# Performance work log

Hardware: AMD Instinct MI355X
Metric: run time of the kernel (lower is better)

The kernel has to match this reference:

```python
import jax, jax.numpy as jnp
import numpy as np

G = 56      # voxel grid side
N = 60000   # active voxels
K = 27      # 3x3x3 kernel offsets
CIN, COUT = 64, 96


def _build_kernel_map(seed=0):
    """Host-side hash-map neighbor search (what spnn does internally).
    Returns in_idx/out_idx of shape (K, N); padded entries have out_idx == N
    (scattered into a trash row) and in_idx == 0 (any valid gather index)."""
    rng = np.random.default_rng(seed)
    flat = rng.choice(G ** 3, size=N, replace=False)
    coords = np.stack(np.unravel_index(flat, (G, G, G)), axis=1)  # (N, 3)
    lut = -np.ones(G ** 3, dtype=np.int64)
    lut[flat] = np.arange(N)
    offs = np.array([(dx, dy, dz) for dx in (-1, 0, 1)
                     for dy in (-1, 0, 1) for dz in (-1, 0, 1)])
    in_idx = np.zeros((K, N), dtype=np.int32)
    out_idx = np.full((K, N), N, dtype=np.int32)
    for k in range(K):
        nb = coords + offs[k]
        ok = np.all((nb >= 0) & (nb < G), axis=1)
        fl = np.clip(nb[:, 0] * G * G + nb[:, 1] * G + nb[:, 2], 0, G ** 3 - 1)
        j = np.where(ok, lut[fl], -1)
        sel = np.nonzero(j >= 0)[0]
        m = sel.shape[0]
        out_idx[k, :m] = sel.astype(np.int32)       # output point i
        in_idx[k, :m] = j[sel].astype(np.int32)     # its neighbor at offset k
    return jnp.asarray(in_idx), jnp.asarray(out_idx)


def setup_inputs() -> dict:
    key = jax.random.key(0)
    ks = jax.random.split(key, 10)
    in_idx, out_idx = _build_kernel_map(0)
    s1 = 1.0 / np.sqrt(K * CIN)
    s2 = 1.0 / np.sqrt(K * COUT)
    return {
        "x":  jax.random.normal(ks[0], (N, CIN), jnp.float32),
        "W1": jax.random.normal(ks[1], (K, CIN, COUT), jnp.float32) * s1,
        "g1": jnp.ones((COUT,), jnp.float32),
        "b1": jnp.zeros((COUT,), jnp.float32),
        "m1": jax.random.normal(ks[2], (COUT,), jnp.float32) * 0.1,
        "v1": jax.random.uniform(ks[3], (COUT,), jnp.float32, 0.5, 1.5),
        "W2": jax.random.normal(ks[4], (K, COUT, COUT), jnp.float32) * s2,
        "g2": jnp.ones((COUT,), jnp.float32),
        "b2": jnp.zeros((COUT,), jnp.float32),
        "m2": jax.random.normal(ks[5], (COUT,), jnp.float32) * 0.1,
        "v2": jax.random.uniform(ks[6], (COUT,), jnp.float32, 0.5, 1.5),
        "Wd": jax.random.normal(ks[7], (CIN, COUT), jnp.float32) / np.sqrt(CIN),
        "gd": jnp.ones((COUT,), jnp.float32),
        "bd": jnp.zeros((COUT,), jnp.float32),
        "md": jax.random.normal(ks[8], (COUT,), jnp.float32) * 0.1,
        "vd": jax.random.uniform(ks[9], (COUT,), jnp.float32, 0.5, 1.5),
        "in_idx": in_idx,
        "out_idx": out_idx,
    }


def _bn(h, g, b, m, v, eps=1e-5):
    return (h - m) * (g * jax.lax.rsqrt(v + eps)) + b


def _sparse_conv(feat, W, in_idx, out_idx):
    # gather -> GEMM -> scatter-add, one pass per kernel offset.
    n = feat.shape[0]
    out = jnp.zeros((n + 1, W.shape[2]), feat.dtype)  # row n = trash row
    for k in range(W.shape[0]):
        out = out.at[out_idx[k]].add(feat[in_idx[k]] @ W[k])
    return out[:n]


def reference(x, W1, g1, b1, m1, v1, W2, g2, b2, m2, v2,
              Wd, gd, bd, md, vd, in_idx, out_idx):
    h = jax.nn.relu(_bn(_sparse_conv(x, W1, in_idx, out_idx), g1, b1, m1, v1))
    h = _bn(_sparse_conv(h, W2, in_idx, out_idx), g2, b2, m2, v2)
    skip = _bn(x @ Wd, gd, bd, md, vd)  # 1x1 conv downsample (inc != outc)
    return jax.nn.relu(h + skip)
```

## Files before the change

### kernel.cpp

```cpp
#include <hip/hip_runtime.h>


typedef __attribute__((ext_vector_type(8))) short bf16x8;
typedef __attribute__((ext_vector_type(4))) float f32x4;
typedef unsigned short u16;

constexpr int K27  = 27;
constexpr int KPAD = 30;
constexpr int CIN  = 64;
constexpr int COUT = 96;
constexpr int W1SZ = 6144;
constexpr int W2SZ = 9216;

#define MFMA __builtin_amdgcn_mfma_f32_16x16x32_bf16

__device__ __forceinline__ u16 f2bf(float f) {
  unsigned u = __float_as_uint(f);
  return (u16)((u + 0x7FFFu + ((u >> 16) & 1u)) >> 16);
}

__device__ __forceinline__ int posf(int c) {
  return ((c >> 2) & 3) * 8 + (c & 3) + ((c >> 4) & 1) * 4;
}

__device__ __forceinline__ bf16x8 ld16(const u16* p) {
  union { bf16x8 f; uint4 u; } r;
  r.u = *reinterpret_cast<const uint4*>(p);
  return r.f;
}

__device__ __forceinline__ void gll(const u16* g, u16* l) {
  __builtin_amdgcn_global_load_lds(
      (const __attribute__((address_space(1))) unsigned int*)g,
      (__attribute__((address_space(3))) unsigned int*)l, 16, 0, 0);
}

__device__ __forceinline__ void stage1(const u16* g, u16* l, int t) {
#pragma unroll
  for (int s = 0; s < 3; ++s) gll(g + s * 2048 + t * 8, l + s * 2048 + t * 8);
}

__device__ __forceinline__ void stage2(const u16* g, u16* l, int t) {
#pragma unroll
  for (int s = 0; s < 4; ++s) gll(g + s * 2048 + t * 8, l + s * 2048 + t * 8);
  if (t < 128) gll(g + 8192 + t * 8, l + 8192 + t * 8);
}

__device__ __forceinline__ int xcd_swz(int bid, int nblk) {
  int q = nblk >> 3, r = nblk & 7;
  int x = bid & 7, i = bid >> 3;
  return (x < r ? x * (q + 1) : r * (q + 1) + (x - r) * q) + i;
}

__global__ void build_nbT(const int* __restrict__ in_idx, const int* __restrict__ out_idx,
                          int* __restrict__ nbT, int N, int N_pad) {
  int t = blockIdx.x * blockDim.x + threadIdx.x;
  if (t >= K27 * N) return;
  int k = t / N;
  int o = out_idx[t];
  if (o < N) nbT[(size_t)k * N_pad + o] = in_idx[t];
}

__global__ void prep_all(
    const float* __restrict__ x, const float* __restrict__ W1,
    const float* __restrict__ W2, const float* __restrict__ Wd,
    const float* g1, const float* b1, const float* m1, const float* v1,
    const float* g2, const float* b2, const float* m2, const float* v2,
    const float* gd, const float* bd, const float* md, const float* vd,
    u16* __restrict__ xbf, u16* __restrict__ W1t, u16* __restrict__ W2t,
    u16* __restrict__ Wdt, float* __restrict__ bnc, u16* __restrict__ hbf, int N) {
  long i = (long)blockIdx.x * blockDim.x + threadIdx.x;
  const long R0 = (long)(N + 1) * CIN;
  const long R1 = (long)K27 * W1SZ;
  const long R2 = (long)K27 * W2SZ;
  const long R3 = (long)CIN * COUT;
  if (i < R0) {
    int c = (int)(i & 63);
    float v = (i < (long)N * CIN) ? x[i] : 0.f;
    xbf[(i & ~63L) + (c & 32) + posf(c & 31)] = f2bf(v);
    return;
  }
  i -= R0;
  if (i < R1) {
    int k = (int)(i / W1SZ), r = (int)(i % W1SZ);
    int f = r >> 9, lane = (r >> 3) & 63, j = r & 7;
    int c = f / 6, n = f % 6, m = lane & 15, g = lane >> 4;
    int co = n * 16 + m;
    int ci = c * 32 + 4 * g + (j & 3) + 16 * (j >> 2);
    W1t[i] = f2bf(W1[((size_t)k * CIN + ci) * COUT + co]);
    return;
  }
  i -= R1;
  if (i < R2) {
    int k = (int)(i / W2SZ), r = (int)(i % W2SZ);
    int f = r >> 9, lane = (r >> 3) & 63, j = r & 7;
    int c = f / 6, n = f % 6, m = lane & 15, g = lane >> 4;
    int co = n * 16 + m;
    int ci = c * 32 + 4 * g + (j & 3) + 16 * (j >> 2);
    W2t[i] = f2bf(W2[((size_t)k * COUT + ci) * COUT + co]);
    return;
  }
  i -= R2;
  if (i < R3) {
    int ci = (int)(i / COUT), co = (int)(i % COUT);
    Wdt[co * CIN + (ci & 32) + posf(ci & 31)] = f2bf(Wd[i]);
    return;
  }
  i -= R3;
  if (i < COUT) {
    int c = (int)i;
    float A1 = g1[c] * rsqrtf(v1[c] + 1e-5f);
    float A2 = g2[c] * rsqrtf(v2[c] + 1e-5f);
    float Ad = gd[c] * rsqrtf(vd[c] + 1e-5f);
    bnc[c]       = A1;
    bnc[96 + c]  = b1[c] - m1[c] * A1;
    bnc[192 + c] = A2;
    bnc[288 + c] = b2[c] - m2[c] * A2 + bd[c] - md[c] * Ad;
    bnc[384 + c] = Ad / A2;
    hbf[(size_t)N * COUT + c] = 0;
  }
}

__global__ __launch_bounds__(256, 2) void conv1_mfma(
    const u16* __restrict__ xbf, const u16* __restrict__ W1t,
    const int* __restrict__ nbT, const float* __restrict__ bnc,
    u16* __restrict__ hbf, int N, int N_pad) {
  __shared__ u16 Blds[2][W1SZ];
  const int t    = threadIdx.x;
  const int lane = t & 63;
  const int m    = lane & 15;
  const int slot = lane >> 4;
  const int so   = slot * 8;
  const int wid  = t >> 6;
  const int wr   = wid >> 1;
  const int wc   = wid & 1;
  const int bswz = xcd_swz(blockIdx.x, gridDim.x);
  const int roww = bswz * 64 + wr * 32;

  f32x4 acc[2][3];
#pragma unroll
  for (int s = 0; s < 2; ++s)
#pragma unroll
    for (int n = 0; n < 3; ++n) acc[s][n] = (f32x4){0.f, 0.f, 0.f, 0.f};

  const int* nbp = nbT + roww + m;

  stage1(W1t, Blds[0], t);
  __builtin_amdgcn_sched_barrier(0);
  int j1a, j1b, j2a, j2b;
  bf16x8 Aa[2][2], Ab[2][2];
  {
    int j0a = nbp[0], j0b = nbp[16];
    j1a = nbp[N_pad];               j1b = nbp[N_pad + 16];
    j2a = nbp[2 * (size_t)N_pad];   j2b = nbp[2 * (size_t)N_pad + 16];
    const u16* pa = xbf + (size_t)(j0a < 0 ? N : j0a) * CIN + so;
    const u16* pb = xbf + (size_t)(j0b < 0 ? N : j0b) * CIN + so;
    Aa[0][0] = ld16(pa); Aa[0][1] = ld16(pa + 32);
    Aa[1][0] = ld16(pb); Aa[1][1] = ld16(pb + 32);
  }
  asm volatile("s_waitcnt vmcnt(6)" ::: "memory");
  __builtin_amdgcn_s_barrier();
  __builtin_amdgcn_sched_barrier(0);

  auto step = [&](int k, bf16x8 (&Ac)[2][2], bf16x8 (&An)[2][2]) {
    const int cur = k & 1;
    stage1(W1t + (size_t)(k + 1) * W1SZ, Blds[cur ^ 1], t);
    __builtin_amdgcn_sched_barrier(0);
    {
      const u16* pa = xbf + (size_t)(j1a < 0 ? N : j1a) * CIN + so;
      const u16* pb = xbf + (size_t)(j1b < 0 ? N : j1b) * CIN + so;
      An[0][0] = ld16(pa); An[0][1] = ld16(pa + 32);
      An[1][0] = ld16(pb); An[1][1] = ld16(pb + 32);
    }
    int j3a = nbp[(size_t)(k + 3) * N_pad];
    int j3b = nbp[(size_t)(k + 3) * N_pad + 16];
    j1a = j2a; j1b = j2b; j2a = j3a; j2b = j3b;
    const u16* Bb = Blds[cur] + wc * 1536 + lane * 8;
#pragma unroll
    for (int c = 0; c < 2; ++c)
#pragma unroll
      for (int nn = 0; nn < 3; ++nn) {
        bf16x8 B = ld16(Bb + (c * 6 + nn) * 512);
        acc[0][nn] = MFMA(Ac[0][c], B, acc[0][nn], 0, 0, 0);
        acc[1][nn] = MFMA(Ac[1][c], B, acc[1][nn], 0, 0, 0);
      }
    asm volatile("s_waitcnt vmcnt(6)" ::: "memory");
    __builtin_amdgcn_s_barrier();
    __builtin_amdgcn_sched_barrier(0);
  };

  for (int kk = 0; kk < K27 - 1; kk += 2) {
    step(kk, Aa, Ab);
    step(kk + 1, Ab, Aa);
  }
  step(K27 - 1, Aa, Ab);
  asm volatile("" :: "v"(Ab[0][0]), "v"(Ab[0][1]), "v"(Ab[1][0]), "v"(Ab[1][1]),
                     "v"(j1a), "v"(j1b), "v"(j2a), "v"(j2b));

  const int pbase = ((m >> 2) << 3) + (m & 3);
#pragma unroll
  for (int nn = 0; nn < 3; ++nn) {
    const int n   = wc * 3 + nn;
    const int col = n * 16 + m;
    const int dcol = (n >> 1) * 32 + pbase + ((n & 1) << 2);
    const float sc = bnc[col], bi = bnc[COUT + col];
#pragma unroll
    for (int s = 0; s < 2; ++s)
#pragma unroll
      for (int r = 0; r < 4; ++r) {
        const int row = roww + s * 16 + slot * 4 + r;
        if (row < N)
          hbf[(size_t)row * COUT + dcol] = f2bf(fmaxf(fmaf(acc[s][nn][r], sc, bi), 0.f));
      }
  }
}

__global__ __launch_bounds__(256, 2) void conv2_mfma(
    const u16* __restrict__ hbf, const u16* __restrict__ W2t,
    const u16* __restrict__ xbf, const u16* __restrict__ Wdt,
    const int* __restrict__ nbT, const float* __restrict__ bnc,
    float* __restrict__ out, int N, int N_pad) {
  __shared__ u16 Blds[2][W2SZ];
  const int t    = threadIdx.x;
  const int lane = t & 63;
  const int m    = lane & 15;
  const int slot = lane >> 4;
  const int so   = slot * 8;
  const int wid  = t >> 6;
  const int wr   = wid >> 1;
  const int wc   = wid & 1;
  const int bswz = xcd_swz(blockIdx.x, gridDim.x);
  const int roww = bswz * 64 + wr * 32;

  f32x4 acc[2][3];
#pragma unroll
  for (int s = 0; s < 2; ++s)
#pragma unroll
    for (int n = 0; n < 3; ++n) acc[s][n] = (f32x4){0.f, 0.f, 0.f, 0.f};

  stage2(W2t, Blds[0], t);
  __builtin_amdgcn_sched_barrier(0);
  {
    int r0 = roww + m, r1 = roww + 16 + m;
    const u16* pa = xbf + (size_t)(r0 < N ? r0 : N) * CIN + so;
    const u16* pb = xbf + (size_t)(r1 < N ? r1 : N) * CIN + so;
    bf16x8 S0a = ld16(pa), S1a = ld16(pa + 32);
    bf16x8 S0b = ld16(pb), S1b = ld16(pb + 32);
#pragma unroll
    for (int nn = 0; nn < 3; ++nn) {
      const int col = (wc * 3 + nn) * 16 + m;
      const u16* wd = Wdt + col * CIN + so;
      bf16x8 B0 = ld16(wd), B1 = ld16(wd + 32);
      acc[0][nn] = MFMA(S0a, B0, acc[0][nn], 0, 0, 0);
      acc[0][nn] = MFMA(S1a, B1, acc[0][nn], 0, 0, 0);
      acc[1][nn] = MFMA(S0b, B0, acc[1][nn], 0, 0, 0);
      acc[1][nn] = MFMA(S1b, B1, acc[1][nn], 0, 0, 0);
    }
#pragma unroll
    for (int nn = 0; nn < 3; ++nn) {
      float rr = bnc[384 + (wc * 3 + nn) * 16 + m];
      acc[0][nn] *= rr;
      acc[1][nn] *= rr;
    }
  }

  const int* nbp = nbT + roww + m;
  int j1a, j1b, j2a, j2b;
  bf16x8 Aa[2][3], Ab[2][3];
  {
    int j0a = nbp[0], j0b = nbp[16];
    j1a = nbp[N_pad];               j1b = nbp[N_pad + 16];
    j2a = nbp[2 * (size_t)N_pad];   j2b = nbp[2 * (size_t)N_pad + 16];
    const u16* pa = hbf + (size_t)(j0a < 0 ? N : j0a) * COUT + so;
    const u16* pb = hbf + (size_t)(j0b < 0 ? N : j0b) * COUT + so;
    Aa[0][0] = ld16(pa); Aa[0][1] = ld16(pa + 32); Aa[0][2] = ld16(pa + 64);
    Aa[1][0] = ld16(pb); Aa[1][1] = ld16(pb + 32); Aa[1][2] = ld16(pb + 64);
  }
  asm volatile("s_waitcnt vmcnt(8)" ::: "memory");
  __builtin_amdgcn_s_barrier();
  __builtin_amdgcn_sched_barrier(0);

  auto step = [&](int k, bf16x8 (&Ac)[2][3], bf16x8 (&An)[2][3]) {
    const int cur = k & 1;
    stage2(W2t + (size_t)(k + 1) * W2SZ, Blds[cur ^ 1], t);
    __builtin_amdgcn_sched_barrier(0);
    {
      const u16* pa = hbf + (size_t)(j1a < 0 ? N : j1a) * COUT + so;
      const u16* pb = hbf + (size_t)(j1b < 0 ? N : j1b) * COUT + so;
      An[0][0] = ld16(pa); An[0][1] = ld16(pa + 32); An[0][2] = ld16(pa + 64);
      An[1][0] = ld16(pb); An[1][1] = ld16(pb + 32); An[1][2] = ld16(pb + 64);
    }
    int j3a = nbp[(size_t)(k + 3) * N_pad];
    int j3b = nbp[(size_t)(k + 3) * N_pad + 16];
    j1a = j2a; j1b = j2b; j2a = j3a; j2b = j3b;
    const u16* Bb = Blds[cur] + wc * 1536 + lane * 8;
#pragma unroll
    for (int c = 0; c < 3; ++c)
#pragma unroll
      for (int nn = 0; nn < 3; ++nn) {
        bf16x8 B = ld16(Bb + (c * 6 + nn) * 512);
        acc[0][nn] = MFMA(Ac[0][c], B, acc[0][nn], 0, 0, 0);
        acc[1][nn] = MFMA(Ac[1][c], B, acc[1][nn], 0, 0, 0);
      }
    asm volatile("s_waitcnt vmcnt(8)" ::: "memory");
    __builtin_amdgcn_s_barrier();
    __builtin_amdgcn_sched_barrier(0);
  };

  for (int kk = 0; kk < K27 - 1; kk += 2) {
    step(kk, Aa, Ab);
    step(kk + 1, Ab, Aa);
  }
  step(K27 - 1, Aa, Ab);
  asm volatile("" :: "v"(Ab[0][0]), "v"(Ab[0][1]), "v"(Ab[0][2]),
                     "v"(Ab[1][0]), "v"(Ab[1][1]), "v"(Ab[1][2]),
                     "v"(j1a), "v"(j1b), "v"(j2a), "v"(j2b));

#pragma unroll
  for (int nn = 0; nn < 3; ++nn) {
    const int col = (wc * 3 + nn) * 16 + m;
    const float sc = bnc[192 + col], bi = bnc[288 + col];
#pragma unroll
    for (int s = 0; s < 2; ++s)
#pragma unroll
      for (int r = 0; r < 4; ++r) {
        const int row = roww + s * 16 + slot * 4 + r;
        if (row < N)
          out[(size_t)row * COUT + col] = fmaxf(fmaf(acc[s][nn][r], sc, bi), 0.f);
      }
  }
}

extern "C" void kernel_launch(void* const* d_in, const int* in_sizes, int n_in,
                              void* d_out, int out_size, void* d_ws, size_t ws_size,
                              hipStream_t stream) {
  const float* x  = (const float*)d_in[0];
  const float* W1 = (const float*)d_in[1];
  const float* g1 = (const float*)d_in[2];
  const float* b1 = (const float*)d_in[3];
  const float* m1 = (const float*)d_in[4];
  const float* v1 = (const float*)d_in[5];
  const float* W2 = (const float*)d_in[6];
  const float* g2 = (const float*)d_in[7];
  const float* b2 = (const float*)d_in[8];
  const float* m2 = (const float*)d_in[9];
  const float* v2 = (const float*)d_in[10];
  const float* Wd = (const float*)d_in[11];
  const float* gd = (const float*)d_in[12];
  const float* bd = (const float*)d_in[13];
  const float* md = (const float*)d_in[14];
  const float* vd = (const float*)d_in[15];
  const int* in_idx  = (const int*)d_in[16];
  const int* out_idx = (const int*)d_in[17];

  const int N  = in_sizes[0] / CIN;
  const int GB = (N + 63) / 64;
  const int N_pad = GB * 64;

  char* ws = (char*)d_ws;
  size_t off = 0;
  auto alloc = [&](size_t bytes) { size_t o = off; off = (off + bytes + 255) & ~(size_t)255; return o; };
  int*   nbT = (int*)(ws + alloc((size_t)KPAD * N_pad * sizeof(int)));
  u16*   xbf = (u16*)(ws + alloc((size_t)(N + 1) * CIN * sizeof(u16)));
  u16*   hbf = (u16*)(ws + alloc((size_t)(N + 1) * COUT * sizeof(u16)));
  u16*   W1t = (u16*)(ws + alloc((size_t)(K27 + 1) * W1SZ * sizeof(u16)));
  u16*   W2t = (u16*)(ws + alloc((size_t)(K27 + 1) * W2SZ * sizeof(u16)));
  u16*   Wdt = (u16*)(ws + alloc((size_t)COUT * CIN * sizeof(u16)));
  float* bnc = (float*)(ws + alloc(5 * 96 * sizeof(float)));

  hipMemsetAsync(nbT, 0xFF, (size_t)KPAD * N_pad * sizeof(int), stream);
  build_nbT<<<(K27 * N + 255) / 256, 256, 0, stream>>>(in_idx, out_idx, nbT, N, N_pad);

  long ptotal = (long)(N + 1) * CIN + (long)K27 * W1SZ + (long)K27 * W2SZ +
                (long)CIN * COUT + COUT;
  prep_all<<<(int)((ptotal + 255) / 256), 256, 0, stream>>>(
      x, W1, W2, Wd, g1, b1, m1, v1, g2, b2, m2, v2, gd, bd, md, vd,
      xbf, W1t, W2t, Wdt, bnc, hbf, N);

  conv1_mfma<<<GB, 256, 0, stream>>>(xbf, W1t, nbT, bnc, hbf, N, N_pad);
  conv2_mfma<<<GB, 256, 0, stream>>>(hbf, W2t, xbf, Wdt, nbT, bnc, (float*)d_out, N, N_pad);
}
```

Measured before the change: 138.8 us.

## Triple-buffer weight staging and deepen gather prefetch in sparse conv kernels

Both conv kernels move from double to triple buffering of the per-offset weight tile in LDS, staging weights two offsets ahead, and prefetch gathered feature rows and neighbor indices one step deeper, with relaxed vmcnt waits. The W2 tiles are padded so every thread issues a uniform five-chunk stage, and the MFMA block is wrapped in s_setprio to favour matrix issue. The aim is to hide more global-load latency behind the MFMAs. The cost is more LDS (which may lower occupancy in conv2) and more live VGPRs.

Result: slower. 157.5 us (+13.4%).

```diff
diff --git a/kernel.cpp b/kernel.cpp
--- a/kernel.cpp
+++ b/kernel.cpp
@@ -5,12 +5,13 @@
 typedef __attribute__((ext_vector_type(4))) float f32x4;
 typedef unsigned short u16;
 
-constexpr int K27  = 27;
-constexpr int KPAD = 30;
-constexpr int CIN  = 64;
-constexpr int COUT = 96;
-constexpr int W1SZ = 6144;
-constexpr int W2SZ = 9216;
+constexpr int K27   = 27;
+constexpr int KPAD  = 32;
+constexpr int CIN   = 64;
+constexpr int COUT  = 96;
+constexpr int W1SZ  = 6144;
+constexpr int W2SZ  = 9216;
+constexpr int W2PAD = 10240;
 
 #define MFMA __builtin_amdgcn_mfma_f32_16x16x32_bf16
 
@@ -39,11 +40,9 @@
 #pragma unroll
   for (int s = 0; s < 3; ++s) gll(g + s * 2048 + t * 8, l + s * 2048 + t * 8);
 }
-
 __device__ __forceinline__ void stage2(const u16* g, u16* l, int t) {
 #pragma unroll
-  for (int s = 0; s < 4; ++s) gll(g + s * 2048 + t * 8, l + s * 2048 + t * 8);
-  if (t < 128) gll(g + 8192 + t * 8, l + 8192 + t * 8);
+  for (int s = 0; s < 5; ++s) gll(g + s * 2048 + t * 8, l + s * 2048 + t * 8);
 }
 
 __device__ __forceinline__ int xcd_swz(int bid, int nblk) {
@@ -97,7 +96,7 @@
     int c = f / 6, n = f % 6, m = lane & 15, g = lane >> 4;
     int co = n * 16 + m;
     int ci = c * 32 + 4 * g + (j & 3) + 16 * (j >> 2);
-    W2t[i] = f2bf(W2[((size_t)k * COUT + ci) * COUT + co]);
+    W2t[(size_t)k * W2PAD + r] = f2bf(W2[((size_t)k * COUT + ci) * COUT + co]);
     return;
   }
   i -= R2;
@@ -125,7 +124,7 @@
     const u16* __restrict__ xbf, const u16* __restrict__ W1t,
     const int* __restrict__ nbT, const float* __restrict__ bnc,
     u16* __restrict__ hbf, int N, int N_pad) {
-  __shared__ u16 Blds[2][W1SZ];
+  __shared__ u16 Blds[3][W1SZ];
   const int t    = threadIdx.x;
   const int lane = t & 63;
   const int m    = lane & 15;
@@ -146,36 +145,44 @@
   const int* nbp = nbT + roww + m;
 
   stage1(W1t, Blds[0], t);
+  stage1(W1t + (size_t)W1SZ, Blds[1], t);
   __builtin_amdgcn_sched_barrier(0);
-  int j1a, j1b, j2a, j2b;
-  bf16x8 Aa[2][2], Ab[2][2];
+  bf16x8 AX[2][2], AY[2][2], AZ[2][2];
+  int J0a, J0b, J1a, J1b, J2a, J2b;
   {
     int j0a = nbp[0], j0b = nbp[16];
-    j1a = nbp[N_pad];               j1b = nbp[N_pad + 16];
-    j2a = nbp[2 * (size_t)N_pad];   j2b = nbp[2 * (size_t)N_pad + 16];
+    int j1a = nbp[N_pad], j1b = nbp[N_pad + 16];
     const u16* pa = xbf + (size_t)(j0a < 0 ? N : j0a) * CIN + so;
     const u16* pb = xbf + (size_t)(j0b < 0 ? N : j0b) * CIN + so;
-    Aa[0][0] = ld16(pa); Aa[0][1] = ld16(pa + 32);
-    Aa[1][0] = ld16(pb); Aa[1][1] = ld16(pb + 32);
-  }
-  asm volatile("s_waitcnt vmcnt(6)" ::: "memory");
+    AX[0][0] = ld16(pa); AX[0][1] = ld16(pa + 32);
+    AX[1][0] = ld16(pb); AX[1][1] = ld16(pb + 32);
+    const u16* qa = xbf + (size_t)(j1a < 0 ? N : j1a) * CIN + so;
+    const u16* qb = xbf + (size_t)(j1b < 0 ? N : j1b) * CIN + so;
+    AY[0][0] = ld16(qa); AY[0][1] = ld16(qa + 32);
+    AY[1][0] = ld16(qb); AY[1][1] = ld16(qb + 32);
+  }
+  J2a = nbp[2 * (size_t)N_pad]; J2b = nbp[2 * (size_t)N_pad + 16];
+  J0a = nbp[3 * (size_t)N_pad]; J0b = nbp[3 * (size_t)N_pad + 16];
+  asm volatile("s_waitcnt vmcnt(12)" ::: "memory");
   __builtin_amdgcn_s_barrier();
   __builtin_amdgcn_sched_barrier(0);
 
-  auto step = [&](int k, bf16x8 (&Ac)[2][2], bf16x8 (&An)[2][2]) {
-    const int cur = k & 1;
-    stage1(W1t + (size_t)(k + 1) * W1SZ, Blds[cur ^ 1], t);
+  auto step = [&](int k, u16* bcur, u16* bdst,
+                  bf16x8 (&Ac)[2][2], bf16x8 (&Ad)[2][2],
+                  int jua, int jub, int& jda, int& jdb) {
+    stage1(W1t + (size_t)(k + 2) * W1SZ, bdst, t);
     __builtin_amdgcn_sched_barrier(0);
     {
-      const u16* pa = xbf + (size_t)(j1a < 0 ? N : j1a) * CIN + so;
-      const u16* pb = xbf + (size_t)(j1b < 0 ? N : j1b) * CIN + so;
-      An[0][0] = ld16(pa); An[0][1] = ld16(pa + 32);
-      An[1][0] = ld16(pb); An[1][1] = ld16(pb + 32);
+      const u16* pa = xbf + (size_t)(jua < 0 ? N : jua) * CIN + so;
+      const u16* pb = xbf + (size_t)(jub < 0 ? N : jub) * CIN + so;
+      Ad[0][0] = ld16(pa); Ad[0][1] = ld16(pa + 32);
+      Ad[1][0] = ld16(pb); Ad[1][1] = ld16(pb + 32);
     }
-    int j3a = nbp[(size_t)(k + 3) * N_pad];
-    int j3b = nbp[(size_t)(k + 3) * N_pad + 16];
-    j1a = j2a; j1b = j2b; j2a = j3a; j2b = j3b;
-    const u16* Bb = Blds[cur] + wc * 1536 + lane * 8;
+    jda = nbp[(size_t)(k + 4) * N_pad];
+    jdb = nbp[(size_t)(k + 4) * N_pad + 16];
+    __builtin_amdgcn_sched_barrier(0);
+    const u16* Bb = bcur + wc * 1536 + lane * 8;
+    __builtin_amdgcn_s_setprio(1);
 #pragma unroll
     for (int c = 0; c < 2; ++c)
 #pragma unroll
@@ -184,18 +191,19 @@
         acc[0][nn] = MFMA(Ac[0][c], B, acc[0][nn], 0, 0, 0);
         acc[1][nn] = MFMA(Ac[1][c], B, acc[1][nn], 0, 0, 0);
       }
-    asm volatile("s_waitcnt vmcnt(6)" ::: "memory");
+    __builtin_amdgcn_s_setprio(0);
+    asm volatile("s_waitcnt vmcnt(15)" ::: "memory");
     __builtin_amdgcn_s_barrier();
     __builtin_amdgcn_sched_barrier(0);
   };
 
-  for (int kk = 0; kk < K27 - 1; kk += 2) {
-    step(kk, Aa, Ab);
-    step(kk + 1, Ab, Aa);
-  }
-  step(K27 - 1, Aa, Ab);
-  asm volatile("" :: "v"(Ab[0][0]), "v"(Ab[0][1]), "v"(Ab[1][0]), "v"(Ab[1][1]),
-                     "v"(j1a), "v"(j1b), "v"(j2a), "v"(j2b));
+  for (int kk = 0; kk < K27; kk += 3) {
+    step(kk + 0, Blds[0], Blds[2], AX, AZ, J2a, J2b, J1a, J1b);
+    step(kk + 1, Blds[1], Blds[0], AY, AX, J0a, J0b, J2a, J2b);
+    step(kk + 2, Blds[2], Blds[1], AZ, AY, J1a, J1b, J0a, J0b);
+  }
+  asm volatile("" :: "v"(AX[0][0]), "v"(AX[1][0]), "v"(AY[0][0]), "v"(AY[1][0]),
+                     "v"(J0a), "v"(J1a), "v"(J2a));
 
   const int pbase = ((m >> 2) << 3) + (m & 3);
 #pragma unroll
@@ -220,7 +228,7 @@
     const u16* __restrict__ xbf, const u16* __restrict__ Wdt,
     const int* __restrict__ nbT, const float* __restrict__ bnc,
     float* __restrict__ out, int N, int N_pad) {
-  __shared__ u16 Blds[2][W2SZ];
+  __shared__ u16 Blds[3][W2PAD];
   const int t    = threadIdx.x;
   const int lane = t & 63;
   const int m    = lane & 15;
@@ -239,6 +247,7 @@
     for (int n = 0; n < 3; ++n) acc[s][n] = (f32x4){0.f, 0.f, 0.f, 0.f};
 
   stage2(W2t, Blds[0], t);
+  stage2(W2t + (size_t)W2PAD, Blds[1], t);
   __builtin_amdgcn_sched_barrier(0);
   {
     int r0 = roww + m, r1 = roww + 16 + m;
@@ -265,35 +274,42 @@
   }
 
   const int* nbp = nbT + roww + m;
-  int j1a, j1b, j2a, j2b;
-  bf16x8 Aa[2][3], Ab[2][3];
+  bf16x8 AX[2][3], AY[2][3], AZ[2][3];
+  int J0a, J0b, J1a, J1b, J2a, J2b;
   {
     int j0a = nbp[0], j0b = nbp[16];
-    j1a = nbp[N_pad];               j1b = nbp[N_pad + 16];
-    j2a = nbp[2 * (size_t)N_pad];   j2b = nbp[2 * (size_t)N_pad + 16];
+    int j1a = nbp[N_pad], j1b = nbp[N_pad + 16];
     const u16* pa = hbf + (size_t)(j0a < 0 ? N : j0a) * COUT + so;
     const u16* pb = hbf + (size_t)(j0b < 0 ? N : j0b) * COUT + so;
-    Aa[0][0] = ld16(pa); Aa[0][1] = ld16(pa + 32); Aa[0][2] = ld16(pa + 64);
-    Aa[1][0] = ld16(pb); Aa[1][1] = ld16(pb + 32); Aa[1][2] = ld16(pb + 64);
-  }
-  asm volatile("s_waitcnt vmcnt(8)" ::: "memory");
+    AX[0][0] = ld16(pa); AX[0][1] = ld16(pa + 32); AX[0][2] = ld16(pa + 64);
+    AX[1][0] = ld16(pb); AX[1][1] = ld16(pb + 32); AX[1][2] = ld16(pb + 64);
+    const u16* qa = hbf + (size_t)(j1a < 0 ? N : j1a) * COUT + so;
+    const u16* qb = hbf + (size_t)(j1b < 0 ? N : j1b) * COUT + so;
+    AY[0][0] = ld16(qa); AY[0][1] = ld16(qa + 32); AY[0][2] = ld16(qa + 64);
+    AY[1][0] = ld16(qb); AY[1][1] = ld16(qb + 32); AY[1][2] = ld16(qb + 64);
+  }
+  J2a = nbp[2 * (size_t)N_pad]; J2b = nbp[2 * (size_t)N_pad + 16];
+  J0a = nbp[3 * (size_t)N_pad]; J0b = nbp[3 * (size_t)N_pad + 16];
+  asm volatile("s_waitcnt vmcnt(16)" ::: "memory");
   __builtin_amdgcn_s_barrier();
   __builtin_amdgcn_sched_barrier(0);
 
-  auto step = [&](int k, bf16x8 (&Ac)[2][3], bf16x8 (&An)[2][3]) {
-    const int cur = k & 1;
-    stage2(W2t + (size_t)(k + 1) * W2SZ, Blds[cur ^ 1], t);
+  auto step = [&](int k, u16* bcur, u16* bdst,
+                  bf16x8 (&Ac)[2][3], bf16x8 (&Ad)[2][3],
+                  int jua, int jub, int& jda, int& jdb) {
+    stage2(W2t + (size_t)(k + 2) * W2PAD, bdst, t);
     __builtin_amdgcn_sched_barrier(0);
     {
-      const u16* pa = hbf + (size_t)(j1a < 0 ? N : j1a) * COUT + so;
-      const u16* pb = hbf + (size_t)(j1b < 0 ? N : j1b) * COUT + so;
-      An[0][0] = ld16(pa); An[0][1] = ld16(pa + 32); An[0][2] = ld16(pa + 64);
-      An[1][0] = ld16(pb); An[1][1] = ld16(pb + 32); An[1][2] = ld16(pb + 64);
+      const u16* pa = hbf + (size_t)(jua < 0 ? N : jua) * COUT + so;
+      const u16* pb = hbf + (size_t)(jub < 0 ? N : jub) * COUT + so;
+      Ad[0][0] = ld16(pa); Ad[0][1] = ld16(pa + 32); Ad[0][2] = ld16(pa + 64);
+      Ad[1][0] = ld16(pb); Ad[1][1] = ld16(pb + 32); Ad[1][2] = ld16(pb + 64);
     }
-    int j3a = nbp[(size_t)(k + 3) * N_pad];
-    int j3b = nbp[(size_t)(k + 3) * N_pad + 16];
-    j1a = j2a; j1b = j2b; j2a = j3a; j2b = j3b;
-    const u16* Bb = Blds[cur] + wc * 1536 + lane * 8;
+    jda = nbp[(size_t)(k + 4) * N_pad];
+    jdb = nbp[(size_t)(k + 4) * N_pad + 16];
+    __builtin_amdgcn_sched_barrier(0);
+    const u16* Bb = bcur + wc * 1536 + lane * 8;
+    __builtin_amdgcn_s_setprio(1);
 #pragma unroll
     for (int c = 0; c < 3; ++c)
 #pragma unroll
@@ -302,19 +318,19 @@
         acc[0][nn] = MFMA(Ac[0][c], B, acc[0][nn], 0, 0, 0);
         acc[1][nn] = MFMA(Ac[1][c], B, acc[1][nn], 0, 0, 0);
       }
-    asm volatile("s_waitcnt vmcnt(8)" ::: "memory");
+    __builtin_amdgcn_s_setprio(0);
+    asm volatile("s_waitcnt vmcnt(21)" ::: "memory");
     __builtin_amdgcn_s_barrier();
     __builtin_amdgcn_sched_barrier(0);
   };
 
-  for (int kk = 0; kk < K27 - 1; kk += 2) {
-    step(kk, Aa, Ab);
-    step(kk + 1, Ab, Aa);
-  }
-  step(K27 - 1, Aa, Ab);
-  asm volatile("" :: "v"(Ab[0][0]), "v"(Ab[0][1]), "v"(Ab[0][2]),
-                     "v"(Ab[1][0]), "v"(Ab[1][1]), "v"(Ab[1][2]),
-                     "v"(j1a), "v"(j1b), "v"(j2a), "v"(j2b));
+  for (int kk = 0; kk < K27; kk += 3) {
+    step(kk + 0, Blds[0], Blds[2], AX, AZ, J2a, J2b, J1a, J1b);
+    step(kk + 1, Blds[1], Blds[0], AY, AX, J0a, J0b, J2a, J2b);
+    step(kk + 2, Blds[2], Blds[1], AZ, AY, J1a, J1b, J0a, J0b);
+  }
+  asm volatile("" :: "v"(AX[0][0]), "v"(AX[1][0]), "v"(AY[0][0]), "v"(AY[1][0]),
+                     "v"(J0a), "v"(J1a), "v"(J2a));
 
 #pragma unroll
   for (int nn = 0; nn < 3; ++nn) {
@@ -363,8 +379,8 @@
   int*   nbT = (int*)(ws + alloc((size_t)KPAD * N_pad * sizeof(int)));
   u16*   xbf = (u16*)(ws + alloc((size_t)(N + 1) * CIN * sizeof(u16)));
   u16*   hbf = (u16*)(ws + alloc((size_t)(N + 1) * COUT * sizeof(u16)));
-  u16*   W1t = (u16*)(ws + alloc((size_t)(K27 + 1) * W1SZ * sizeof(u16)));
-  u16*   W2t = (u16*)(ws + alloc((size_t)(K27 + 1) * W2SZ * sizeof(u16)));
+  u16*   W1t = (u16*)(ws + alloc((size_t)(K27 + 2) * W1SZ * sizeof(u16)));
+  u16*   W2t = (u16*)(ws + alloc((size_t)(K27 + 2) * W2PAD * sizeof(u16)));
   u16*   Wdt = (u16*)(ws + alloc((size_t)COUT * CIN * sizeof(u16)));
   float* bnc = (float*)(ws + alloc(5 * 96 * sizeof(float)));
 
```

## Replace LDS-staged weights with single-wave blocks reading weights from global

Applied to the files above, without the earlier changes.

Both conv kernels change from 256-thread blocks that double-buffer each offset's weight slice in shared memory via global_load_lds to one-wave blocks of 32 rows. Each wave now covers all 96 output columns and loads weights straight from global/L2 each step, with no barriers or LDS. This removes block-wide synchronisation and LDS staging, at the cost of more redundant weight traffic through the cache and twice the accumulator registers per wave. KPAD grows to 32 so the index prefetch at k+3 stays in bounds.

New measurement: 171.7 us. +23.7%, slower.

```diff
diff --git a/kernel.cpp b/kernel.cpp
--- a/kernel.cpp
+++ b/kernel.cpp
@@ -6,7 +6,7 @@
 typedef unsigned short u16;
 
 constexpr int K27  = 27;
-constexpr int KPAD = 30;
+constexpr int KPAD = 32;
 constexpr int CIN  = 64;
 constexpr int COUT = 96;
 constexpr int W1SZ = 6144;
@@ -27,23 +27,6 @@
   union { bf16x8 f; uint4 u; } r;
   r.u = *reinterpret_cast<const uint4*>(p);
   return r.f;
-}
-
-__device__ __forceinline__ void gll(const u16* g, u16* l) {
-  __builtin_amdgcn_global_load_lds(
-      (const __attribute__((address_space(1))) unsigned int*)g,
-      (__attribute__((address_space(3))) unsigned int*)l, 16, 0, 0);
-}
-
-__device__ __forceinline__ void stage1(const u16* g, u16* l, int t) {
-#pragma unroll
-  for (int s = 0; s < 3; ++s) gll(g + s * 2048 + t * 8, l + s * 2048 + t * 8);
-}
-
-__device__ __forceinline__ void stage2(const u16* g, u16* l, int t) {
-#pragma unroll
-  for (int s = 0; s < 4; ++s) gll(g + s * 2048 + t * 8, l + s * 2048 + t * 8);
-  if (t < 128) gll(g + 8192 + t * 8, l + 8192 + t * 8);
 }
 
 __device__ __forceinline__ int xcd_swz(int bid, int nblk) {
@@ -121,51 +104,37 @@
   }
 }
 
-__global__ __launch_bounds__(256, 2) void conv1_mfma(
+__global__ __launch_bounds__(64, 4) void conv1_mfma(
     const u16* __restrict__ xbf, const u16* __restrict__ W1t,
     const int* __restrict__ nbT, const float* __restrict__ bnc,
     u16* __restrict__ hbf, int N, int N_pad) {
-  __shared__ u16 Blds[2][W1SZ];
-  const int t    = threadIdx.x;
-  const int lane = t & 63;
+  const int lane = threadIdx.x & 63;
   const int m    = lane & 15;
   const int slot = lane >> 4;
   const int so   = slot * 8;
-  const int wid  = t >> 6;
-  const int wr   = wid >> 1;
-  const int wc   = wid & 1;
-  const int bswz = xcd_swz(blockIdx.x, gridDim.x);
-  const int roww = bswz * 64 + wr * 32;
-
-  f32x4 acc[2][3];
+  const int roww = xcd_swz(blockIdx.x, gridDim.x) * 32;
+
+  f32x4 acc[2][6];
 #pragma unroll
   for (int s = 0; s < 2; ++s)
 #pragma unroll
-    for (int n = 0; n < 3; ++n) acc[s][n] = (f32x4){0.f, 0.f, 0.f, 0.f};
+    for (int n = 0; n < 6; ++n) acc[s][n] = (f32x4){0.f, 0.f, 0.f, 0.f};
 
   const int* nbp = nbT + roww + m;
 
-  stage1(W1t, Blds[0], t);
-  __builtin_amdgcn_sched_barrier(0);
   int j1a, j1b, j2a, j2b;
   bf16x8 Aa[2][2], Ab[2][2];
   {
     int j0a = nbp[0], j0b = nbp[16];
-    j1a = nbp[N_pad];               j1b = nbp[N_pad + 16];
-    j2a = nbp[2 * (size_t)N_pad];   j2b = nbp[2 * (size_t)N_pad + 16];
+    j1a = nbp[N_pad];             j1b = nbp[N_pad + 16];
+    j2a = nbp[2 * (size_t)N_pad]; j2b = nbp[2 * (size_t)N_pad + 16];
     const u16* pa = xbf + (size_t)(j0a < 0 ? N : j0a) * CIN + so;
     const u16* pb = xbf + (size_t)(j0b < 0 ? N : j0b) * CIN + so;
     Aa[0][0] = ld16(pa); Aa[0][1] = ld16(pa + 32);
     Aa[1][0] = ld16(pb); Aa[1][1] = ld16(pb + 32);
   }
-  asm volatile("s_waitcnt vmcnt(6)" ::: "memory");
-  __builtin_amdgcn_s_barrier();
-  __builtin_amdgcn_sched_barrier(0);
 
   auto step = [&](int k, bf16x8 (&Ac)[2][2], bf16x8 (&An)[2][2]) {
-    const int cur = k & 1;
-    stage1(W1t + (size_t)(k + 1) * W1SZ, Blds[cur ^ 1], t);
-    __builtin_amdgcn_sched_barrier(0);
     {
       const u16* pa = xbf + (size_t)(j1a < 0 ? N : j1a) * CIN + so;
       const u16* pb = xbf + (size_t)(j1b < 0 ? N : j1b) * CIN + so;
@@ -175,18 +144,15 @@
     int j3a = nbp[(size_t)(k + 3) * N_pad];
     int j3b = nbp[(size_t)(k + 3) * N_pad + 16];
     j1a = j2a; j1b = j2b; j2a = j3a; j2b = j3b;
-    const u16* Bb = Blds[cur] + wc * 1536 + lane * 8;
+    const u16* wk = W1t + (size_t)k * W1SZ + lane * 8;
 #pragma unroll
     for (int c = 0; c < 2; ++c)
 #pragma unroll
-      for (int nn = 0; nn < 3; ++nn) {
-        bf16x8 B = ld16(Bb + (c * 6 + nn) * 512);
-        acc[0][nn] = MFMA(Ac[0][c], B, acc[0][nn], 0, 0, 0);
-        acc[1][nn] = MFMA(Ac[1][c], B, acc[1][nn], 0, 0, 0);
+      for (int n = 0; n < 6; ++n) {
+        bf16x8 B = ld16(wk + (c * 6 + n) * 512);
+        acc[0][n] = MFMA(Ac[0][c], B, acc[0][n], 0, 0, 0);
+        acc[1][n] = MFMA(Ac[1][c], B, acc[1][n], 0, 0, 0);
       }
-    asm volatile("s_waitcnt vmcnt(6)" ::: "memory");
-    __builtin_amdgcn_s_barrier();
-    __builtin_amdgcn_sched_barrier(0);
   };
 
   for (int kk = 0; kk < K27 - 1; kk += 2) {
@@ -194,14 +160,11 @@
     step(kk + 1, Ab, Aa);
   }
   step(K27 - 1, Aa, Ab);
-  asm volatile("" :: "v"(Ab[0][0]), "v"(Ab[0][1]), "v"(Ab[1][0]), "v"(Ab[1][1]),
-                     "v"(j1a), "v"(j1b), "v"(j2a), "v"(j2b));
 
   const int pbase = ((m >> 2) << 3) + (m & 3);
 #pragma unroll
-  for (int nn = 0; nn < 3; ++nn) {
-    const int n   = wc * 3 + nn;
-    const int col = n * 16 + m;
+  for (int n = 0; n < 6; ++n) {
+    const int col  = n * 16 + m;
     const int dcol = (n >> 1) * 32 + pbase + ((n & 1) << 2);
     const float sc = bnc[col], bi = bnc[COUT + col];
 #pragma unroll
@@ -210,36 +173,28 @@
       for (int r = 0; r < 4; ++r) {
         const int row = roww + s * 16 + slot * 4 + r;
         if (row < N)
-          hbf[(size_t)row * COUT + dcol] = f2bf(fmaxf(fmaf(acc[s][nn][r], sc, bi), 0.f));
+          hbf[(size_t)row * COUT + dcol] = f2bf(fmaxf(fmaf(acc[s][n][r], sc, bi), 0.f));
       }
   }
 }
 
-__global__ __launch_bounds__(256, 2) void conv2_mfma(
+__global__ __launch_bounds__(64, 3) void conv2_mfma(
     const u16* __restrict__ hbf, const u16* __restrict__ W2t,
     const u16* __restrict__ xbf, const u16* __restrict__ Wdt,
     const int* __restrict__ nbT, const float* __restrict__ bnc,
     float* __restrict__ out, int N, int N_pad) {
-  __shared__ u16 Blds[2][W2SZ];
-  const int t    = threadIdx.x;
-  const int lane = t & 63;
+  const int lane = threadIdx.x & 63;
   const int m    = lane & 15;
   const int slot = lane >> 4;
   const int so   = slot * 8;
-  const int wid  = t >> 6;
-  const int wr   = wid >> 1;
-  const int wc   = wid & 1;
-  const int bswz = xcd_swz(blockIdx.x, gridDim.x);
-  const int roww = bswz * 64 + wr * 32;
-
-  f32x4 acc[2][3];
+  const int roww = xcd_swz(blockIdx.x, gridDim.x) * 32;
+
+  f32x4 acc[2][6];
 #pragma unroll
   for (int s = 0; s < 2; ++s)
 #pragma unroll
-    for (int n = 0; n < 3; ++n) acc[s][n] = (f32x4){0.f, 0.f, 0.f, 0.f};
-
-  stage2(W2t, Blds[0], t);
-  __builtin_amdgcn_sched_barrier(0);
+    for (int n = 0; n < 6; ++n) acc[s][n] = (f32x4){0.f, 0.f, 0.f, 0.f};
+
   {
     int r0 = roww + m, r1 = roww + 16 + m;
     const u16* pa = xbf + (size_t)(r0 < N ? r0 : N) * CIN + so;
@@ -247,20 +202,20 @@
     bf16x8 S0a = ld16(pa), S1a = ld16(pa + 32);
     bf16x8 S0b = ld16(pb), S1b = ld16(pb + 32);
 #pragma unroll
-    for (int nn = 0; nn < 3; ++nn) {
-      const int col = (wc * 3 + nn) * 16 + m;
+    for (int n = 0; n < 6; ++n) {
+      const int col = n * 16 + m;
       const u16* wd = Wdt + col * CIN + so;
       bf16x8 B0 = ld16(wd), B1 = ld16(wd + 32);
-      acc[0][nn] = MFMA(S0a, B0, acc[0][nn], 0, 0, 0);
-      acc[0][nn] = MFMA(S1a, B1, acc[0][nn], 0, 0, 0);
-      acc[1][nn] = MFMA(S0b, B0, acc[1][nn], 0, 0, 0);
-      acc[1][nn] = MFMA(S1b, B1, acc[1][nn], 0, 0, 0);
+      acc[0][n] = MFMA(S0a, B0, acc[0][n], 0, 0, 0);
+      acc[0][n] = MFMA(S1a, B1, acc[0][n], 0, 0, 0);
+      acc[1][n] = MFMA(S0b, B0, acc[1][n], 0, 0, 0);
+      acc[1][n] = MFMA(S1b, B1, acc[1][n], 0, 0, 0);
     }
 #pragma unroll
-    for (int nn = 0; nn < 3; ++nn) {
-      float rr = bnc[384 + (wc * 3 + nn) * 16 + m];
-      acc[0][nn] *= rr;
-      acc[1][nn] *= rr;
+    for (int n = 0; n < 6; ++n) {
+      float rr = bnc[384 + n * 16 + m];
+      acc[0][n] *= rr;
+      acc[1][n] *= rr;
     }
   }
 
@@ -269,21 +224,15 @@
   bf16x8 Aa[2][3], Ab[2][3];
   {
     int j0a = nbp[0], j0b = nbp[16];
-    j1a = nbp[N_pad];               j1b = nbp[N_pad + 16];
-    j2a = nbp[2 * (size_t)N_pad];   j2b = nbp[2 * (size_t)N_pad + 16];
+    j1a = nbp[N_pad];             j1b = nbp[N_pad + 16];
+    j2a = nbp[2 * (size_t)N_pad]; j2b = nbp[2 * (size_t)N_pad + 16];
     const u16* pa = hbf + (size_t)(j0a < 0 ? N : j0a) * COUT + so;
     const u16* pb = hbf + (size_t)(j0b < 0 ? N : j0b) * COUT + so;
     Aa[0][0] = ld16(pa); Aa[0][1] = ld16(pa + 32); Aa[0][2] = ld16(pa + 64);
     Aa[1][0] = ld16(pb); Aa[1][1] = ld16(pb + 32); Aa[1][2] = ld16(pb + 64);
   }
-  asm volatile("s_waitcnt vmcnt(8)" ::: "memory");
-  __builtin_amdgcn_s_barrier();
-  __builtin_amdgcn_sched_barrier(0);
 
   auto step = [&](int k, bf16x8 (&Ac)[2][3], bf16x8 (&An)[2][3]) {
-    const int cur = k & 1;
-    stage2(W2t + (size_t)(k + 1) * W2SZ, Blds[cur ^ 1], t);
-    __builtin_amdgcn_sched_barrier(0);
     {
       const u16* pa = hbf + (size_t)(j1a < 0 ? N : j1a) * COUT + so;
       const u16* pb = hbf + (size_t)(j1b < 0 ? N : j1b) * COUT + so;
@@ -293,18 +242,15 @@
     int j3a = nbp[(size_t)(k + 3) * N_pad];
     int j3b = nbp[(size_t)(k + 3) * N_pad + 16];
     j1a = j2a; j1b = j2b; j2a = j3a; j2b = j3b;
-    const u16* Bb = Blds[cur] + wc * 1536 + lane * 8;
+    const u16* wk = W2t + (size_t)k * W2SZ + lane * 8;
 #pragma unroll
     for (int c = 0; c < 3; ++c)
 #pragma unroll
-      for (int nn = 0; nn < 3; ++nn) {
-        bf16x8 B = ld16(Bb + (c * 6 + nn) * 512);
-        acc[0][nn] = MFMA(Ac[0][c], B, acc[0][nn], 0, 0, 0);
-        acc[1][nn] = MFMA(Ac[1][c], B, acc[1][nn], 0, 0, 0);
+      for (int n = 0; n < 6; ++n) {
+        bf16x8 B = ld16(wk + (c * 6 + n) * 512);
+        acc[0][n] = MFMA(Ac[0][c], B, acc[0][n], 0, 0, 0);
+        acc[1][n] = MFMA(Ac[1][c], B, acc[1][n], 0, 0, 0);
       }
-    asm volatile("s_waitcnt vmcnt(8)" ::: "memory");
-    __builtin_amdgcn_s_barrier();
-    __builtin_amdgcn_sched_barrier(0);
   };
 
   for (int kk = 0; kk < K27 - 1; kk += 2) {
@@ -312,13 +258,10 @@
     step(kk + 1, Ab, Aa);
   }
   step(K27 - 1, Aa, Ab);
-  asm volatile("" :: "v"(Ab[0][0]), "v"(Ab[0][1]), "v"(Ab[0][2]),
-                     "v"(Ab[1][0]), "v"(Ab[1][1]), "v"(Ab[1][2]),
-                     "v"(j1a), "v"(j1b), "v"(j2a), "v"(j2b));
-
-#pragma unroll
-  for (int nn = 0; nn < 3; ++nn) {
-    const int col = (wc * 3 + nn) * 16 + m;
+
+#pragma unroll
+  for (int n = 0; n < 6; ++n) {
+    const int col = n * 16 + m;
     const float sc = bnc[192 + col], bi = bnc[288 + col];
 #pragma unroll
     for (int s = 0; s < 2; ++s)
@@ -326,7 +269,7 @@
       for (int r = 0; r < 4; ++r) {
         const int row = roww + s * 16 + slot * 4 + r;
         if (row < N)
-          out[(size_t)row * COUT + col] = fmaxf(fmaf(acc[s][nn][r], sc, bi), 0.f);
+          out[(size_t)row * COUT + col] = fmaxf(fmaf(acc[s][n][r], sc, bi), 0.f);
       }
   }
 }
@@ -353,9 +296,9 @@
   const int* in_idx  = (const int*)d_in[16];
   const int* out_idx = (const int*)d_in[17];
 
-  const int N  = in_sizes[0] / CIN;
-  const int GB = (N + 63) / 64;
-  const int N_pad = GB * 64;
+  const int N    = in_sizes[0] / CIN;
+  const int GB32 = (N + 31) / 32;
+  const int N_pad = ((N + 63) / 64) * 64;
 
   char* ws = (char*)d_ws;
   size_t off = 0;
@@ -363,8 +306,8 @@
   int*   nbT = (int*)(ws + alloc((size_t)KPAD * N_pad * sizeof(int)));
   u16*   xbf = (u16*)(ws + alloc((size_t)(N + 1) * CIN * sizeof(u16)));
   u16*   hbf = (u16*)(ws + alloc((size_t)(N + 1) * COUT * sizeof(u16)));
-  u16*   W1t = (u16*)(ws + alloc((size_t)(K27 + 1) * W1SZ * sizeof(u16)));
-  u16*   W2t = (u16*)(ws + alloc((size_t)(K27 + 1) * W2SZ * sizeof(u16)));
+  u16*   W1t = (u16*)(ws + alloc((size_t)K27 * W1SZ * sizeof(u16)));
+  u16*   W2t = (u16*)(ws + alloc((size_t)K27 * W2SZ * sizeof(u16)));
   u16*   Wdt = (u16*)(ws + alloc((size_t)COUT * CIN * sizeof(u16)));
   float* bnc = (float*)(ws + alloc(5 * 96 * sizeof(float)));
 
@@ -377,6 +320,6 @@
       x, W1, W2, Wd, g1, b1, m1, v1, g2, b2, m2, v2, gd, bd, md, vd,
       xbf, W1t, W2t, Wdt, bnc, hbf, N);
 
-  conv1_mfma<<<GB, 256, 0, stream>>>(xbf, W1t, nbT, bnc, hbf, N, N_pad);
-  conv2_mfma<<<GB, 256, 0, stream>>>(hbf, W2t, xbf, Wdt, nbT, bnc, (float*)d_out, N, N_pad);
-}
+  conv1_mfma<<<GB32, 64, 0, stream>>>(xbf, W1t, nbT, bnc, hbf, N, N_pad);
+  conv2_mfma<<<GB32, 64, 0, stream>>>(hbf, W2t, xbf, Wdt, nbT, bnc, (float*)d_out, N, N_pad);
+}
```
